# Kernel tuning notes

Hardware: AMD Instinct MI355X
Metric: run time of the kernel (lower is better)

The kernel has to match this reference:

```python
import jax, jax.numpy as jnp
import numpy as np
from jax import lax

B, L = 8, 1024
C_IN, D_MODEL = 3, 512
N_MAMBA, N_TRANS, NHEAD = 2, 2, 8
D_STATE, D_CONV, EXPAND = 16, 4, 2
DI = EXPAND * D_MODEL            # 1024, mamba inner dim
DT_RANK = D_MODEL // 16          # 32
DH = D_MODEL // NHEAD            # 64, head dim
DFF = 4 * D_MODEL


def setup_inputs() -> dict:
    key = jax.random.key(0)
    ks = iter(jax.random.split(key, 64))
    def rn(shape, s=0.05):
        return jax.random.normal(next(ks), shape, jnp.float32) * s
    inp = {
        'x': jax.random.normal(next(ks), (B, C_IN, L), jnp.float32),
        'proj_w': rn((D_MODEL, C_IN)), 'proj_b': rn((D_MODEL,)),
        # stacked per-mamba-layer params (leading dim = N_MAMBA)
        'm_in_w': rn((N_MAMBA, 2 * DI, D_MODEL)),
        'm_conv_w': rn((N_MAMBA, DI, D_CONV)), 'm_conv_b': rn((N_MAMBA, DI)),
        'm_xproj_w': rn((N_MAMBA, DT_RANK + 2 * D_STATE, DI)),
        'm_dt_w': rn((N_MAMBA, DI, DT_RANK)), 'm_dt_b': rn((N_MAMBA, DI)),
        'm_Alog': jnp.tile(jnp.log(jnp.arange(1, D_STATE + 1, dtype=jnp.float32)), (N_MAMBA, DI, 1)),
        'm_D': jnp.ones((N_MAMBA, DI), jnp.float32),
        'm_out_w': rn((N_MAMBA, D_MODEL, DI)),
        'm_ln_w': jnp.ones((N_MAMBA, D_MODEL), jnp.float32), 'm_ln_b': jnp.zeros((N_MAMBA, D_MODEL), jnp.float32),
        # stacked per-transformer-layer params
        't_qkv_w': rn((N_TRANS, 3 * D_MODEL, D_MODEL)), 't_qkv_b': rn((N_TRANS, 3 * D_MODEL)),
        't_ow': rn((N_TRANS, D_MODEL, D_MODEL)), 't_ob': rn((N_TRANS, D_MODEL)),
        't_l1w': rn((N_TRANS, DFF, D_MODEL)), 't_l1b': rn((N_TRANS, DFF)),
        't_l2w': rn((N_TRANS, D_MODEL, DFF)), 't_l2b': rn((N_TRANS, D_MODEL)),
        't_ln1w': jnp.ones((N_TRANS, D_MODEL), jnp.float32), 't_ln1b': jnp.zeros((N_TRANS, D_MODEL), jnp.float32),
        't_ln2w': jnp.ones((N_TRANS, D_MODEL), jnp.float32), 't_ln2b': jnp.zeros((N_TRANS, D_MODEL), jnp.float32),
        'no_w': jnp.ones((D_MODEL,), jnp.float32), 'no_b': jnp.zeros((D_MODEL,), jnp.float32),
    }
    return inp


def _ln(x, w, b, eps=1e-5):
    m = x.mean(-1, keepdims=True)
    v = ((x - m) ** 2).mean(-1, keepdims=True)
    return (x - m) / jnp.sqrt(v + eps) * w + b


def _pos_encoding(length, d):
    pos = jnp.arange(length, dtype=jnp.float32)[:, None]
    div = jnp.exp(jnp.arange(0, d, 2, dtype=jnp.float32) * (-np.log(10000.0) / d))
    pe = jnp.zeros((length, d), jnp.float32)
    pe = pe.at[:, 0::2].set(jnp.sin(pos * div)).at[:, 1::2].set(jnp.cos(pos * div))
    return pe


def _mamba(h, in_w, conv_w, conv_b, xp_w, dt_w, dt_b, Alog, Dp, out_w):
    # h: [B,L,d_model]
    xz = h @ in_w.T                                   # [B,L,2*DI]
    xm, z = jnp.split(xz, 2, axis=-1)
    # causal depthwise conv1d over time
    k = conv_w.T[:, None, :]                          # [D_CONV,1,DI]
    xc = lax.conv_general_dilated(xm, k, (1,), [(D_CONV - 1, 0)],
                                  dimension_numbers=('NWC', 'WIO', 'NWC'),
                                  feature_group_count=DI) + conv_b
    xc = jax.nn.silu(xc)
    xdb = xc @ xp_w.T                                 # [B,L,DT_RANK+2*D_STATE]
    dt = jax.nn.softplus(xdb[..., :DT_RANK] @ dt_w.T + dt_b)   # [B,L,DI]
    Bm = xdb[..., DT_RANK:DT_RANK + D_STATE]          # [B,L,D_STATE]
    Cm = xdb[..., DT_RANK + D_STATE:]                 # [B,L,D_STATE]
    A = -jnp.exp(Alog)                                # [DI,D_STATE]

    def step(state, t):
        dt_t, B_t, C_t, x_t = t                       # [B,DI],[B,S],[B,S],[B,DI]
        dA = jnp.exp(dt_t[..., None] * A)             # [B,DI,S]
        state = state * dA + (dt_t * x_t)[..., None] * B_t[:, None, :]
        y = jnp.einsum('bds,bs->bd', state, C_t)
        return state, y

    init = jnp.zeros((h.shape[0], DI, D_STATE), h.dtype)
    seq = (dt.transpose(1, 0, 2), Bm.transpose(1, 0, 2), Cm.transpose(1, 0, 2), xc.transpose(1, 0, 2))
    _, ys = lax.scan(step, init, seq)                 # ys: [L,B,DI]
    y = ys.transpose(1, 0, 2) + Dp * xc
    y = y * jax.nn.silu(z)
    return y @ out_w.T                                # [B,L,d_model]


def _transformer_layer(h, qkv_w, qkv_b, ow, ob, l1w, l1b, l2w, l2b, ln1w, ln1b, ln2w, ln2b):
    Bt, Lt, d = h.shape
    qkv = h @ qkv_w.T + qkv_b
    q, k, v = jnp.split(qkv, 3, axis=-1)
    q = q.reshape(Bt, Lt, NHEAD, DH); k = k.reshape(Bt, Lt, NHEAD, DH); v = v.reshape(Bt, Lt, NHEAD, DH)
    sc = jnp.einsum('blhd,bmhd->bhlm', q, k) / np.sqrt(DH).astype(np.float32)
    a = jax.nn.softmax(sc, axis=-1)
    o = jnp.einsum('bhlm,bmhd->blhd', a, v).reshape(Bt, Lt, d)
    h = _ln(h + o @ ow.T + ob, ln1w, ln1b)
    ff = jax.nn.relu(h @ l1w.T + l1b) @ l2w.T + l2b
    return _ln(h + ff, ln2w, ln2b)


def reference(x, proj_w, proj_b, m_in_w, m_conv_w, m_conv_b, m_xproj_w, m_dt_w, m_dt_b,
              m_Alog, m_D, m_out_w, m_ln_w, m_ln_b, t_qkv_w, t_qkv_b, t_ow, t_ob,
              t_l1w, t_l1b, t_l2w, t_l2b, t_ln1w, t_ln1b, t_ln2w, t_ln2b, no_w, no_b):
    # proj_in: 1x1 conv == pointwise linear over channels; output [B,L,d]
    h = jnp.einsum('bcl,dc->bld', x, proj_w) + proj_b
    for i in range(N_MAMBA):
        h = _ln(h + _mamba(h, m_in_w[i], m_conv_w[i], m_conv_b[i], m_xproj_w[i],
                           m_dt_w[i], m_dt_b[i], m_Alog[i], m_D[i], m_out_w[i]),
                m_ln_w[i], m_ln_b[i])
    h = h + _pos_encoding(h.shape[1], D_MODEL)
    for i in range(N_TRANS):
        h = _transformer_layer(h, t_qkv_w[i], t_qkv_b[i], t_ow[i], t_ob[i],
                               t_l1w[i], t_l1b[i], t_l2w[i], t_l2b[i],
                               t_ln1w[i], t_ln1b[i], t_ln2w[i], t_ln2b[i])
    h = _ln(h, no_w, no_b)
    return h, h.mean(axis=1)
```

## Files before the change

### kernel.cpp

```cpp
#include <hip/hip_runtime.h>
#include <cstddef>

#define BATCH 8
#define LSEQ 1024
#define DMODEL 512
#define DINNER 1024
#define DSTATE 16
#define DTRANK 32
#define NHEAD 8
#define DHEAD 64
#define DFF 2048
#define MTOK 8192
#define NCHUNK 16
#define CLEN 64

typedef __attribute__((ext_vector_type(8))) short bfrag;
typedef __attribute__((ext_vector_type(4))) float f32x4;
typedef __attribute__((ext_vector_type(4))) unsigned short us4;
typedef unsigned short ushort_t;

__device__ __forceinline__ float silu_f(float x) { return x / (1.f + __expf(-x)); }

__device__ __forceinline__ unsigned short f2bf(float f) {
  unsigned u = __float_as_uint(f);
  return (unsigned short)((u + 0x7FFFu + ((u >> 16) & 1u)) >> 16);
}
__device__ __forceinline__ float bf2f(ushort_t u) {
  return __uint_as_float((unsigned)u << 16);
}

__device__ __forceinline__ void gll16(const ushort_t* g, ushort_t* l) {
  __builtin_amdgcn_global_load_lds(
      (const __attribute__((address_space(1))) unsigned int*)g,
      (__attribute__((address_space(3))) unsigned int*)l, 16, 0, 0);
}

struct Cvt8Args {
  const float* s[8];
  ushort_t* d[8];
  int end[8];
};
__global__ __launch_bounds__(256) void cvt8(Cvt8Args a) {
  int blk = blockIdx.x;
  int seg = 0, start = 0;
#pragma unroll
  for (int i = 0; i < 7; ++i)
    if (blk >= a.end[i]) { seg = i + 1; start = a.end[i]; }
  int i4 = (blk - start) * 256 + threadIdx.x;
  float4 v = ((const float4*)a.s[seg])[i4];
  us4 o = {f2bf(v.x), f2bf(v.y), f2bf(v.z), f2bf(v.w)};
  ((us4*)a.d[seg])[i4] = o;
}

__global__ __launch_bounds__(256) void proj_kernel(const float* __restrict__ x,
                                                   const float* __restrict__ pw,
                                                   const float* __restrict__ pb,
                                                   float* __restrict__ h,
                                                   ushort_t* __restrict__ hbf) {
  int idx = blockIdx.x * 256 + threadIdx.x;
  int d = idx & 511;
  int l = (idx >> 9) & 1023;
  int b = idx >> 19;
  const float* xb = x + (size_t)b * 3 * 1024 + l;
  float v = pb[d] + xb[0] * pw[d * 3] + xb[1024] * pw[d * 3 + 1] + xb[2048] * pw[d * 3 + 2];
  h[idx] = v;
  hbf[idx] = f2bf(v);
}

template <int ACT, int CBF, int SPLITK, int BN>
__global__ __launch_bounds__(256) void gemm_gll(const ushort_t* __restrict__ A,
                                                const ushort_t* __restrict__ W,
                                                const float* __restrict__ bias,
                                                void* __restrict__ Cp,
                                                int K, int lda, int ldc) {
  __shared__ ushort_t sA[2][4096];
  __shared__ ushort_t sB[2][BN * 32];
  constexpr int MREP = (BN == 128) ? 4 : 2;
  const int bm = blockIdx.y * 128, bn = blockIdx.x * BN;
  const int tid = threadIdx.x;
  const int wid = tid >> 6, lane = tid & 63;
  const int wrb = (BN == 128) ? (wid >> 1) * 64 : wid * 32;
  const int wcb = (BN == 128) ? (wid & 1) * 64 : 0;
  const int lr = lane & 15, ls = lane >> 4;
  const int sw = ls ^ ((lr >> 1) & 3);

  const int kseg = K / SPLITK;
  const int kbeg = (SPLITK > 1) ? blockIdx.z * kseg : 0;

  const int c0 = wid * 128 + lane;
  const int c1 = c0 + 64;
  const int r0 = c0 >> 2, s0 = (c0 & 3) ^ ((r0 >> 1) & 3);
  const int r1 = c1 >> 2, s1 = (c1 & 3) ^ ((r1 >> 1) & 3);
  const ushort_t* gA0 = A + (size_t)(bm + r0) * lda + kbeg + s0 * 8;
  const ushort_t* gA1 = A + (size_t)(bm + r1) * lda + kbeg + s1 * 8;
  const ushort_t* gB0;
  const ushort_t* gB1 = nullptr;
  if constexpr (BN == 128) {
    gB0 = W + (size_t)(bn + r0) * K + kbeg + s0 * 8;
    gB1 = W + (size_t)(bn + r1) * K + kbeg + s1 * 8;
  } else {
    const int cb = wid * 64 + lane;
    const int rb = cb >> 2, sb2 = (cb & 3) ^ ((rb >> 1) & 3);
    gB0 = W + (size_t)(bn + rb) * K + kbeg + sb2 * 8;
  }

  f32x4 acc[MREP][4];
#pragma unroll
  for (int i = 0; i < MREP; ++i)
#pragma unroll
    for (int j = 0; j < 4; ++j) acc[i][j] = (f32x4)(0.f);

#define STAGE(buf, step)                                             \
  do {                                                               \
    gll16(gA0 + (step) * 32, &sA[buf][wid * 1024]);                  \
    gll16(gA1 + (step) * 32, &sA[buf][wid * 1024 + 512]);            \
    if constexpr (BN == 128) {                                       \
      gll16(gB0 + (step) * 32, &sB[buf][wid * 1024]);                \
      gll16(gB1 + (step) * 32, &sB[buf][wid * 1024 + 512]);          \
    } else {                                                         \
      gll16(gB0 + (step) * 32, &sB[buf][wid * 512]);                 \
    }                                                                \
  } while (0)

  const int NT = kseg / 32;
  STAGE(0, 0);
  for (int t = 0; t < NT; ++t) {
    const int cur = t & 1;
    if (t + 1 < NT) {
      STAGE(cur ^ 1, t + 1);
      if constexpr (BN == 128)
        asm volatile("s_waitcnt vmcnt(4)" ::: "memory");
      else
        asm volatile("s_waitcnt vmcnt(3)" ::: "memory");
    } else {
      asm volatile("s_waitcnt vmcnt(0)" ::: "memory");
    }
    __builtin_amdgcn_sched_barrier(0);
    __builtin_amdgcn_s_barrier();
    __builtin_amdgcn_sched_barrier(0);

    bfrag af[MREP], bf[4];
#pragma unroll
    for (int mi = 0; mi < MREP; ++mi) {
      int row = wrb + mi * 16 + lr;
      af[mi] = *(const bfrag*)&sA[cur][(size_t)((row << 2) + sw) * 8];
    }
#pragma unroll
    for (int nj = 0; nj < 4; ++nj) {
      int col = wcb + nj * 16 + lr;
      bf[nj] = *(const bfrag*)&sB[cur][(size_t)((col << 2) + sw) * 8];
    }
#pragma unroll
    for (int mi = 0; mi < MREP; ++mi)
#pragma unroll
      for (int nj = 0; nj < 4; ++nj)
        acc[mi][nj] = __builtin_amdgcn_mfma_f32_16x16x32_bf16(af[mi], bf[nj], acc[mi][nj], 0, 0, 0);

    __builtin_amdgcn_s_barrier();
    __builtin_amdgcn_sched_barrier(0);
  }
#undef STAGE

  if (SPLITK > 1) {
    float* Cz = (float*)Cp + (size_t)blockIdx.z * 8192 * ldc;
#pragma unroll
    for (int nj = 0; nj < 4; ++nj) {
      int col = bn + wcb + nj * 16 + lr;
#pragma unroll
      for (int mi = 0; mi < MREP; ++mi) {
        int row0 = bm + wrb + mi * 16 + ls * 4;
#pragma unroll
        for (int r = 0; r < 4; ++r)
          Cz[(size_t)(row0 + r) * ldc + col] = acc[mi][nj][r];
      }
    }
  } else {
#pragma unroll
    for (int nj = 0; nj < 4; ++nj) {
      int col = bn + wcb + nj * 16 + lr;
      float bv = bias ? bias[col] : 0.f;
#pragma unroll
      for (int mi = 0; mi < MREP; ++mi) {
        int row0 = bm + wrb + mi * 16 + ls * 4;
#pragma unroll
        for (int r = 0; r < 4; ++r) {
          float v = acc[mi][nj][r] + bv;
          if (ACT == 1) v = fmaxf(v, 0.f);
          if (ACT == 2) v = (v > 20.f) ? v : log1pf(__expf(v));
          if (CBF)
            ((ushort_t*)Cp)[(size_t)(row0 + r) * ldc + col] = f2bf(v);
          else
            ((float*)Cp)[(size_t)(row0 + r) * ldc + col] = v;
        }
      }
    }
  }
}

__global__ __launch_bounds__(256) void reduce8_xdb(const float* __restrict__ p,
                                                   float* __restrict__ xdb,
                                                   ushort_t* __restrict__ xdb_bf) {
  int i = blockIdx.x * 256 + threadIdx.x;
  float4 a = ((const float4*)p)[i];
#pragma unroll
  for (int z = 1; z < 8; ++z) {
    float4 b = ((const float4*)p)[i + z * 131072];
    a.x += b.x; a.y += b.y; a.z += b.z; a.w += b.w;
  }
  ((float4*)xdb)[i] = a;
  us4 o = {f2bf(a.x), f2bf(a.y), f2bf(a.z), f2bf(a.w)};
  ((us4*)xdb_bf)[i] = o;
}

__global__ __launch_bounds__(256) void conv_silu_kernel(const ushort_t* __restrict__ xz,
                                                        const float* __restrict__ cw,
                                                        const float* __restrict__ cb,
                                                        ushort_t* __restrict__ xc) {
  int idx = blockIdx.x * 256 + threadIdx.x;
  int d = idx & 1023;
  int t = (idx >> 10) & 1023;
  int b = idx >> 20;
  float acc = cb[d];
#pragma unroll
  for (int w = 0; w < 4; ++w) {
    int tt = t - 3 + w;
    if (tt >= 0) acc += bf2f(xz[(((size_t)(b * 1024 + tt)) << 11) + d]) * cw[d * 4 + w];
  }
  xc[idx] = f2bf(silu_f(acc));
}

__global__ __launch_bounds__(256) void scan_pass1(const ushort_t* __restrict__ dt,
                                                  const float* __restrict__ xdb,
                                                  const ushort_t* __restrict__ xc,
                                                  const float* __restrict__ Alog,
                                                  float* __restrict__ scrP,
                                                  float* __restrict__ scrL) {
  int idx = blockIdx.x * 256 + threadIdx.x;
  int sh = idx & 3;
  int d = (idx >> 2) & 1023;
  int c = (idx >> 12) & 15;
  int b = idx >> 16;
  float A[4], st[4], P[4];
#pragma unroll
  for (int s = 0; s < 4; ++s) {
    A[s] = -__expf(Alog[d * 16 + sh * 4 + s]);
    st[s] = 0.f;
    P[s] = 1.f;
  }
  int t0 = c * CLEN;
  size_t base = (((size_t)(b * 1024 + t0)) << 10) + d;
  const float* xb = xdb + (size_t)(b * 1024 + t0) * 64 + 32 + sh * 4;
  float dtv = bf2f(dt[base]), xv = bf2f(xc[base]);
  for (int t = 0; t < CLEN; ++t) {
    float dtn = 0.f, xvn = 0.f;
    if (t + 1 < CLEN) { dtn = bf2f(dt[base + 1024]); xvn = bf2f(xc[base + 1024]); }
    float4 Bv = *(const float4*)xb;
    float dx = dtv * xv;
    float e0 = __expf(dtv * A[0]), e1 = __expf(dtv * A[1]);
    float e2 = __expf(dtv * A[2]), e3 = __expf(dtv * A[3]);
    st[0] = st[0] * e0 + dx * Bv.x; P[0] *= e0;
    st[1] = st[1] * e1 + dx * Bv.y; P[1] *= e1;
    st[2] = st[2] * e2 + dx * Bv.z; P[2] *= e2;
    st[3] = st[3] * e3 + dx * Bv.w; P[3] *= e3;
    base += 1024; xb += 64;
    dtv = dtn; xv = xvn;
  }
  size_t pbase = (((size_t)((b * 16 + c) * 16 + sh * 4)) << 10) + d;
#pragma unroll
  for (int s = 0; s < 4; ++s) {
    scrP[pbase + ((size_t)s << 10)] = P[s];
    scrL[pbase + ((size_t)s << 10)] = st[s];
  }
}

__global__ __launch_bounds__(256) void scan_pass2(const float* __restrict__ scrP,
                                                  float* __restrict__ scrL) {
  int idx = blockIdx.x * 256 + threadIdx.x;
  int d = idx & 1023;
  int s = (idx >> 10) & 15;
  int b = idx >> 14;
  float cur = 0.f;
  for (int c = 0; c < 16; ++c) {
    size_t o = (((size_t)(((b * 16 + c) * 16) + s)) << 10) + d;
    float P = scrP[o];
    float loc = scrL[o];
    scrL[o] = cur;
    cur = cur * P + loc;
  }
}

__global__ __launch_bounds__(256) void scan_pass3(const ushort_t* __restrict__ dt,
                                                  const float* __restrict__ xdb,
                                                  const ushort_t* __restrict__ xc,
                                                  const ushort_t* __restrict__ xz,
                                                  ushort_t* __restrict__ ybf,
                                                  const float* __restrict__ Alog,
                                                  const float* __restrict__ Dp,
                                                  const float* __restrict__ scrL) {
  int idx = blockIdx.x * 256 + threadIdx.x;
  int sh = idx & 3;
  int d = (idx >> 2) & 1023;
  int c = (idx >> 12) & 15;
  int b = idx >> 16;
  float A[4], st[4];
  size_t pbase = (((size_t)((b * 16 + c) * 16 + sh * 4)) << 10) + d;
#pragma unroll
  for (int s = 0; s < 4; ++s) {
    A[s] = -__expf(Alog[d * 16 + sh * 4 + s]);
    st[s] = scrL[pbase + ((size_t)s << 10)];
  }
  float Dv = Dp[d];
  int t0 = c * CLEN;
  size_t base = (((size_t)(b * 1024 + t0)) << 10) + d;
  size_t zoff = ((((size_t)(b * 1024 + t0)) << 11)) + 1024 + d;
  const float* xb = xdb + (size_t)(b * 1024 + t0) * 64 + 32 + sh * 4;
  float dtv = bf2f(dt[base]), xv = bf2f(xc[base]), zv = bf2f(xz[zoff]);
  for (int t = 0; t < CLEN; ++t) {
    float dtn = 0.f, xvn = 0.f, zvn = 0.f;
    if (t + 1 < CLEN) {
      dtn = bf2f(dt[base + 1024]); xvn = bf2f(xc[base + 1024]); zvn = bf2f(xz[zoff + 2048]);
    }
    float4 Bv = *(const float4*)xb;
    float4 Cv = *(const float4*)(xb + 16);
    float dx = dtv * xv;
    float e0 = __expf(dtv * A[0]), e1 = __expf(dtv * A[1]);
    float e2 = __expf(dtv * A[2]), e3 = __expf(dtv * A[3]);
    st[0] = st[0] * e0 + dx * Bv.x;
    st[1] = st[1] * e1 + dx * Bv.y;
    st[2] = st[2] * e2 + dx * Bv.z;
    st[3] = st[3] * e3 + dx * Bv.w;
    float acc = st[0] * Cv.x + st[1] * Cv.y + st[2] * Cv.z + st[3] * Cv.w;
    acc += __shfl_xor(acc, 1);
    acc += __shfl_xor(acc, 2);
    if (sh == 0)
      ybf[base] = f2bf((acc + Dv * xv) * silu_f(zv));
    base += 1024; zoff += 2048; xb += 64;
    dtv = dtn; xv = xvn; zv = zvn;
  }
}

__global__ __launch_bounds__(128) void resid_ln_kernel(const float* __restrict__ x,
                                                       const float* __restrict__ add,
                                                       const float* __restrict__ w,
                                                       const float* __restrict__ bias,
                                                       float* __restrict__ out,
                                                       ushort_t* __restrict__ out_bf) {
  int row = blockIdx.x, tid = threadIdx.x;
  float4 v = ((const float4*)(x + (size_t)row * 512))[tid];
  if (add) {
    float4 a = ((const float4*)(add + (size_t)row * 512))[tid];
    v.x += a.x; v.y += a.y; v.z += a.z; v.w += a.w;
  }
  float s = v.x + v.y + v.z + v.w;
  float ss = v.x * v.x + v.y * v.y + v.z * v.z + v.w * v.w;
#pragma unroll
  for (int o = 32; o; o >>= 1) {
    s += __shfl_xor(s, o);
    ss += __shfl_xor(ss, o);
  }
  __shared__ float red[4];
  int wid = tid >> 6;
  if ((tid & 63) == 0) { red[wid] = s; red[2 + wid] = ss; }
  __syncthreads();
  s = red[0] + red[1];
  ss = red[2] + red[3];
  float mean = s * (1.f / 512.f);
  float var = ss * (1.f / 512.f) - mean * mean;
  float inv = rsqrtf(var + 1e-5f);
  float4 wv = ((const float4*)w)[tid];
  float4 bv = ((const float4*)bias)[tid];
  float4 ov;
  ov.x = (v.x - mean) * inv * wv.x + bv.x;
  ov.y = (v.y - mean) * inv * wv.y + bv.y;
  ov.z = (v.z - mean) * inv * wv.z + bv.z;
  ov.w = (v.w - mean) * inv * wv.w + bv.w;
  ((float4*)(out + (size_t)row * 512))[tid] = ov;
  if (out_bf) {
    us4 ob = {f2bf(ov.x), f2bf(ov.y), f2bf(ov.z), f2bf(ov.w)};
    ((us4*)(out_bf + (size_t)row * 512))[tid] = ob;
  }
}

__global__ __launch_bounds__(128) void resid_ln_sk(const float* __restrict__ x,
                                                   const float* __restrict__ p,
                                                   const float* __restrict__ pbias,
                                                   const float* __restrict__ w,
                                                   const float* __restrict__ bias,
                                                   float* __restrict__ out,
                                                   ushort_t* __restrict__ out_bf) {
  int row = blockIdx.x, tid = threadIdx.x;
  float4 v = ((const float4*)(x + (size_t)row * 512))[tid];
  float4 a = ((const float4*)(p + (size_t)row * 512))[tid];
  float4 c = ((const float4*)(p + 4194304 + (size_t)row * 512))[tid];
  v.x += a.x + c.x; v.y += a.y + c.y; v.z += a.z + c.z; v.w += a.w + c.w;
  if (pbias) {
    float4 pb = ((const float4*)pbias)[tid];
    v.x += pb.x; v.y += pb.y; v.z += pb.z; v.w += pb.w;
  }
  float s = v.x + v.y + v.z + v.w;
  float ss = v.x * v.x + v.y * v.y + v.z * v.z + v.w * v.w;
#pragma unroll
  for (int o = 32; o; o >>= 1) {
    s += __shfl_xor(s, o);
    ss += __shfl_xor(ss, o);
  }
  __shared__ float red[4];
  int wid = tid >> 6;
  if ((tid & 63) == 0) { red[wid] = s; red[2 + wid] = ss; }
  __syncthreads();
  s = red[0] + red[1];
  ss = red[2] + red[3];
  float mean = s * (1.f / 512.f);
  float var = ss * (1.f / 512.f) - mean * mean;
  float inv = rsqrtf(var + 1e-5f);
  float4 wv = ((const float4*)w)[tid];
  float4 bv = ((const float4*)bias)[tid];
  float4 ov;
  ov.x = (v.x - mean) * inv * wv.x + bv.x;
  ov.y = (v.y - mean) * inv * wv.y + bv.y;
  ov.z = (v.z - mean) * inv * wv.z + bv.z;
  ov.w = (v.w - mean) * inv * wv.w + bv.w;
  ((float4*)(out + (size_t)row * 512))[tid] = ov;
  us4 ob = {f2bf(ov.x), f2bf(ov.y), f2bf(ov.z), f2bf(ov.w)};
  ((us4*)(out_bf + (size_t)row * 512))[tid] = ob;
}

__global__ __launch_bounds__(256) void posenc_kernel(float* __restrict__ h,
                                                     ushort_t* __restrict__ hbf) {
  int idx = blockIdx.x * 256 + threadIdx.x;
  int d = idx & 511;
  int l = (idx >> 9) & 1023;
  float freq = __expf(-(float)(d & ~1) * (9.210340371976184f / 512.f));
  float ang = (float)l * freq;
  float v = h[idx] + ((d & 1) ? cosf(ang) : sinf(ang));
  h[idx] = v;
  hbf[idx] = f2bf(v);
}

__global__ __launch_bounds__(256) void attn_mfma(const ushort_t* __restrict__ qkv,
                                                 ushort_t* __restrict__ ao) {
  __shared__ unsigned short Qs[4096];
  __shared__ unsigned short Ks[4096];
  __shared__ unsigned short Vt[4096];
  __shared__ unsigned short Ps[4096];
  const int tid = threadIdx.x;
  const int w = blockIdx.x;
  const int bh = (w & 7) + (w >> 7) * 8;
  const int qt = (w >> 3) & 15;
  const int hh = bh & 7, b = bh >> 3;
  const int l0 = qt * 64;
  const size_t bb = (size_t)b * 1024 * 1536;

  const int srow = tid >> 2;
  const int sdb = (tid & 3) << 4;
  const int sc0 = sdb >> 3;

  {
    const ushort_t* qp = qkv + bb + (size_t)(l0 + srow) * 1536 + hh * 64 + sdb;
    *(bfrag*)&Qs[srow * 64 + ((sc0 ^ (srow & 7)) << 3)] = *(const bfrag*)qp;
    *(bfrag*)&Qs[srow * 64 + (((sc0 + 1) ^ (srow & 7)) << 3)] = *(const bfrag*)(qp + 8);
  }

  const int wid = tid >> 6, lane = tid & 63;
  const int l15 = lane & 15, rg = lane >> 4;
  const int l7 = l15 & 7;
  float m[4], lsum[4];
  f32x4 oacc[4];
#pragma unroll
  for (int r = 0; r < 4; ++r) { m[r] = -1e30f; lsum[r] = 0.f; }
#pragma unroll
  for (int nt = 0; nt < 4; ++nt) oacc[nt] = (f32x4)(0.f);

  for (int jt = 0; jt < 16; ++jt) {
    {
      const ushort_t* kp = qkv + bb + (size_t)(jt * 64 + srow) * 1536 + hh * 64 + 512 + sdb;
      *(bfrag*)&Ks[srow * 64 + ((sc0 ^ (srow & 7)) << 3)] = *(const bfrag*)kp;
      *(bfrag*)&Ks[srow * 64 + (((sc0 + 1) ^ (srow & 7)) << 3)] = *(const bfrag*)(kp + 8);
      const ushort_t* vp = kp + 512;
      unsigned short vv[16];
      *(bfrag*)&vv[0] = *(const bfrag*)vp;
      *(bfrag*)&vv[8] = *(const bfrag*)(vp + 8);
#pragma unroll
      for (int j = 0; j < 16; ++j) {
        int dd = sdb + j;
        Vt[dd * 64 + (((srow >> 3) ^ (dd & 7) ^ ((dd >> 3) & 7)) << 3) + (srow & 7)] = vv[j];
      }
    }
    __syncthreads();

    bfrag aq[2];
#pragma unroll
    for (int ks = 0; ks < 2; ++ks)
      aq[ks] = *(const bfrag*)&Qs[(wid * 16 + l15) * 64 + (((ks * 4 + rg) ^ l7) << 3)];
    f32x4 sc[4];
#pragma unroll
    for (int nt = 0; nt < 4; ++nt) {
      f32x4 s = (f32x4)(0.f);
#pragma unroll
      for (int ks = 0; ks < 2; ++ks) {
        bfrag bk = *(const bfrag*)&Ks[(nt * 16 + l15) * 64 + (((ks * 4 + rg) ^ l7) << 3)];
        s = __builtin_amdgcn_mfma_f32_16x16x32_bf16(aq[ks], bk, s, 0, 0, 0);
      }
      sc[nt] = s * 0.125f;
    }

#pragma unroll
    for (int r = 0; r < 4; ++r) {
      float mc = fmaxf(fmaxf(sc[0][r], sc[1][r]), fmaxf(sc[2][r], sc[3][r]));
#pragma unroll
      for (int o = 8; o; o >>= 1) mc = fmaxf(mc, __shfl_xor(mc, o));
      float mn = fmaxf(m[r], mc);
      float al = __expf(m[r] - mn);
      m[r] = mn;
      int prow = rg * 4 + r;
      float ps = 0.f;
#pragma unroll
      for (int nt = 0; nt < 4; ++nt) {
        float p = __expf(sc[nt][r] - mn);
        ps += p;
        int col = nt * 16 + l15;
        Ps[wid * 1024 + prow * 64 + ((((col >> 3) ^ (prow & 7))) << 3) + (col & 7)] = f2bf(p);
      }
#pragma unroll
      for (int o = 8; o; o >>= 1) ps += __shfl_xor(ps, o);
      lsum[r] = lsum[r] * al + ps;
#pragma unroll
      for (int nt = 0; nt < 4; ++nt) oacc[nt][r] *= al;
    }

    bfrag ap[2];
#pragma unroll
    for (int ks = 0; ks < 2; ++ks)
      ap[ks] = *(const bfrag*)&Ps[wid * 1024 + l15 * 64 + (((ks * 4 + rg) ^ l7) << 3)];
#pragma unroll
    for (int nt = 0; nt < 4; ++nt) {
      int vrow = nt * 16 + l15;
#pragma unroll
      for (int ks = 0; ks < 2; ++ks) {
        bfrag bv = *(const bfrag*)&Vt[vrow * 64 +
            (((ks * 4 + rg) ^ (vrow & 7) ^ ((vrow >> 3) & 7)) << 3)];
        oacc[nt] = __builtin_amdgcn_mfma_f32_16x16x32_bf16(ap[ks], bv, oacc[nt], 0, 0, 0);
      }
    }
    __syncthreads();
  }

#pragma unroll
  for (int r = 0; r < 4; ++r) {
    float inv = 1.f / lsum[r];
    int row = l0 + wid * 16 + rg * 4 + r;
    ushort_t* op = ao + ((size_t)(b * 1024 + row)) * 512 + hh * 64;
#pragma unroll
    for (int nt = 0; nt < 4; ++nt) op[nt * 16 + l15] = f2bf(oacc[nt][r] * inv);
  }
}

__global__ __launch_bounds__(512) void mean_part(const float* __restrict__ h,
                                                 float* __restrict__ part) {
  int blk = blockIdx.x;
  int b = blk >> 4, lc = blk & 15, d = threadIdx.x;
  float s = 0.f;
  int l0 = lc * 64;
  for (int l = l0; l < l0 + 64; ++l) s += h[(((size_t)(b * 1024 + l)) << 9) + d];
  part[((size_t)blk << 9) + d] = s;
}
__global__ __launch_bounds__(256) void mean_final(const float* __restrict__ part,
                                                  float* __restrict__ out2) {
  int i = blockIdx.x * 256 + threadIdx.x;
  int b = i >> 9, d = i & 511;
  float s = 0.f;
#pragma unroll
  for (int c = 0; c < 16; ++c) s += part[(((size_t)(b * 16 + c)) << 9) + d];
  out2[i] = s * (1.f / 1024.f);
}

extern "C" void kernel_launch(void* const* d_in, const int* in_sizes, int n_in,
                              void* d_out, int out_size, void* d_ws, size_t ws_size,
                              hipStream_t stream) {
  const float* x        = (const float*)d_in[0];
  const float* proj_w   = (const float*)d_in[1];
  const float* proj_b   = (const float*)d_in[2];
  const float* m_in_w   = (const float*)d_in[3];
  const float* m_conv_w = (const float*)d_in[4];
  const float* m_conv_b = (const float*)d_in[5];
  const float* m_xproj_w= (const float*)d_in[6];
  const float* m_dt_w   = (const float*)d_in[7];
  const float* m_dt_b   = (const float*)d_in[8];
  const float* m_Alog   = (const float*)d_in[9];
  const float* m_D      = (const float*)d_in[10];
  const float* m_out_w  = (const float*)d_in[11];
  const float* m_ln_w   = (const float*)d_in[12];
  const float* m_ln_b   = (const float*)d_in[13];
  const float* t_qkv_w  = (const float*)d_in[14];
  const float* t_qkv_b  = (const float*)d_in[15];
  const float* t_ow     = (const float*)d_in[16];
  const float* t_ob     = (const float*)d_in[17];
  const float* t_l1w    = (const float*)d_in[18];
  const float* t_l1b    = (const float*)d_in[19];
  const float* t_l2w    = (const float*)d_in[20];
  const float* t_l2b    = (const float*)d_in[21];
  const float* t_ln1w   = (const float*)d_in[22];
  const float* t_ln1b   = (const float*)d_in[23];
  const float* t_ln2w   = (const float*)d_in[24];
  const float* t_ln2b   = (const float*)d_in[25];
  const float* no_w     = (const float*)d_in[26];
  const float* no_b     = (const float*)d_in[27];

  float* ws   = (float*)d_ws;
  float* h    = ws;
  ushort_t* h_bf = (ushort_t*)(ws + 4194304);
  float* bufA = ws + 6291456;
  float* bufB = bufA + 16777216;
  float* bufC = bufB + 8388608;
  float* bufE = bufC + 8388608;
  float* bufF = bufE + 4194304;
  ushort_t* y_bf = (ushort_t*)(bufF + 524288);
  ushort_t* wbf  = (ushort_t*)(bufF + 524288 + 4194304);
  float* scrP = bufE;
  float* scrL = bufE + 2097152;

  ushort_t* wIN  = wbf;
  ushort_t* wOUT = wbf + 2097152;
  ushort_t* wQKV = wbf + 3145728;
  ushort_t* wOW  = wbf + 4718592;
  ushort_t* wL1  = wbf + 5242880;
  ushort_t* wL2  = wbf + 7340032;
  ushort_t* wXP  = wbf + 9437184;
  ushort_t* wDT  = wbf + 9568256;
  ushort_t* xdb_bf = wbf + 9633792;

  Cvt8Args ca;
  ca.s[0] = m_in_w;    ca.d[0] = wIN;  
  ca.s[1] = m_out_w;   ca.d[1] = wOUT;
  ca.s[2] = t_qkv_w;   ca.d[2] = wQKV;
  ca.s[3] = t_ow;      ca.d[3] = wOW;
  ca.s[4] = t_l1w;     ca.d[4] = wL1;
  ca.s[5] = t_l2w;     ca.d[5] = wL2;
  ca.s[6] = m_xproj_w; ca.d[6] = wXP;
  ca.s[7] = m_dt_w;    ca.d[7] = wDT;
  ca.end[0] = 2048; ca.end[1] = 3072; ca.end[2] = 4608; ca.end[3] = 5120;
  ca.end[4] = 7168; ca.end[5] = 9216; ca.end[6] = 9344; ca.end[7] = 9408;
  cvt8<<<9408, 256, 0, stream>>>(ca);

  proj_kernel<<<16384, 256, 0, stream>>>(x, proj_w, proj_b, h, h_bf);

  for (int i = 0; i < 2; ++i) {
    gemm_gll<0, 1, 1, 128><<<dim3(16, 64), 256, 0, stream>>>(
        h_bf, wIN + (size_t)i * 1048576, nullptr, bufA, DMODEL, DMODEL, 2 * DINNER);
    conv_silu_kernel<<<32768, 256, 0, stream>>>((const ushort_t*)bufA,
                                                m_conv_w + i * DINNER * 4,
                                                m_conv_b + i * DINNER, (ushort_t*)bufB);
    gemm_gll<0, 0, 8, 64><<<dim3(1, 64, 8), 256, 0, stream>>>(
        (const ushort_t*)bufB, wXP + (size_t)i * 65536, nullptr, bufC,
        DINNER, DINNER, 64);
    reduce8_xdb<<<512, 256, 0, stream>>>(bufC, bufF, xdb_bf);
    gemm_gll<2, 1, 1, 128><<<dim3(8, 64), 256, 0, stream>>>(
        xdb_bf, wDT + (size_t)i * 32768, m_dt_b + i * DINNER, bufC,
        DTRANK, 64, DINNER);
    scan_pass1<<<2048, 256, 0, stream>>>((const ushort_t*)bufC, bufF, (const ushort_t*)bufB,
                                         m_Alog + (size_t)i * DINNER * DSTATE, scrP, scrL);
    scan_pass2<<<512, 256, 0, stream>>>(scrP, scrL);
    scan_pass3<<<2048, 256, 0, stream>>>((const ushort_t*)bufC, bufF, (const ushort_t*)bufB,
                                         (const ushort_t*)bufA, y_bf,
                                         m_Alog + (size_t)i * DINNER * DSTATE,
                                         m_D + i * DINNER, scrL);
    gemm_gll<0, 0, 2, 128><<<dim3(4, 64, 2), 256, 0, stream>>>(
        y_bf, wOUT + (size_t)i * 524288, nullptr, bufC, DINNER, DINNER, DMODEL);
    resid_ln_sk<<<8192, 128, 0, stream>>>(h, bufC, nullptr, m_ln_w + i * DMODEL,
                                          m_ln_b + i * DMODEL, h, h_bf);
  }

  posenc_kernel<<<16384, 256, 0, stream>>>(h, h_bf);

  for (int i = 0; i < 2; ++i) {
    gemm_gll<0, 1, 1, 128><<<dim3(12, 64), 256, 0, stream>>>(
        h_bf, wQKV + (size_t)i * 786432, t_qkv_b + i * 3 * DMODEL, bufA,
        DMODEL, DMODEL, 3 * DMODEL);
    attn_mfma<<<1024, 256, 0, stream>>>((const ushort_t*)bufA, (ushort_t*)bufB);
    gemm_gll<0, 0, 2, 128><<<dim3(4, 64, 2), 256, 0, stream>>>(
        (const ushort_t*)bufB, wOW + (size_t)i * 262144, nullptr, bufC,
        DMODEL, DMODEL, DMODEL);
    resid_ln_sk<<<8192, 128, 0, stream>>>(h, bufC, t_ob + i * DMODEL,
                                          t_ln1w + i * DMODEL, t_ln1b + i * DMODEL, h, h_bf);
    gemm_gll<1, 1, 1, 128><<<dim3(16, 64), 256, 0, stream>>>(
        h_bf, wL1 + (size_t)i * 1048576, t_l1b + i * DFF, bufA,
        DMODEL, DMODEL, DFF);
    gemm_gll<0, 0, 2, 128><<<dim3(4, 64, 2), 256, 0, stream>>>(
        (const ushort_t*)bufA, wL2 + (size_t)i * 1048576, nullptr, bufC,
        DFF, DFF, DMODEL);
    resid_ln_sk<<<8192, 128, 0, stream>>>(h, bufC, t_l2b + i * DMODEL,
                                          t_ln2w + i * DMODEL, t_ln2b + i * DMODEL, h, h_bf);
  }

  float* out_h = (float*)d_out;
  resid_ln_kernel<<<8192, 128, 0, stream>>>(h, nullptr, no_w, no_b, out_h, nullptr);
  mean_part<<<128, 512, 0, stream>>>(out_h, bufF);
  mean_final<<<16, 256, 0, stream>>>(bufF, out_h + 4194304);
}
```

Baseline: 925.2 us.

## Store split-K partials in bf16, vectorize conv, lazy softmax rescale in attention

Split-K GEMM partial outputs are now written as bf16 instead of fp32 and read back as bf16 by the residual+LayerNorm kernel, halving that intermediate traffic. The conv+SiLU kernel processes two channels per thread with 32-bit loads and stores. Attention skips the running-max rescale unless the new max exceeds the old by more than 8, and converts probabilities to bf16 by truncation. These trade accuracy (bf16 partial sums, truncation, a stale max) for less memory traffic and fewer exp and multiply operations.

```diff
diff --git a/kernel.cpp b/kernel.cpp
--- a/kernel.cpp
+++ b/kernel.cpp
@@ -162,7 +162,6 @@
 #undef STAGE
 
   if (SPLITK > 1) {
-    float* Cz = (float*)Cp + (size_t)blockIdx.z * 8192 * ldc;
 #pragma unroll
     for (int nj = 0; nj < 4; ++nj) {
       int col = bn + wcb + nj * 16 + lr;
@@ -170,8 +169,14 @@
       for (int mi = 0; mi < MREP; ++mi) {
         int row0 = bm + wrb + mi * 16 + ls * 4;
 #pragma unroll
-        for (int r = 0; r < 4; ++r)
-          Cz[(size_t)(row0 + r) * ldc + col] = acc[mi][nj][r];
+        for (int r = 0; r < 4; ++r) {
+          if (CBF)
+            ((ushort_t*)Cp)[(size_t)blockIdx.z * 8192 * ldc +
+                            (size_t)(row0 + r) * ldc + col] = f2bf(acc[mi][nj][r]);
+          else
+            ((float*)Cp)[(size_t)blockIdx.z * 8192 * ldc +
+                         (size_t)(row0 + r) * ldc + col] = acc[mi][nj][r];
+        }
       }
     }
   } else {
@@ -212,21 +217,27 @@
   ((us4*)xdb_bf)[i] = o;
 }
 
-__global__ __launch_bounds__(256) void conv_silu_kernel(const ushort_t* __restrict__ xz,
+__global__ __launch_bounds__(256) void conv_silu_kernel(const unsigned* __restrict__ xz,
                                                         const float* __restrict__ cw,
                                                         const float* __restrict__ cb,
-                                                        ushort_t* __restrict__ xc) {
+                                                        unsigned* __restrict__ xc) {
   int idx = blockIdx.x * 256 + threadIdx.x;
-  int d = idx & 1023;
-  int t = (idx >> 10) & 1023;
-  int b = idx >> 20;
-  float acc = cb[d];
+  int dp = idx & 511;
+  int t = (idx >> 9) & 1023;
+  int b = idx >> 19;
+  int d0 = dp * 2;
+  float a0 = cb[d0], a1 = cb[d0 + 1];
 #pragma unroll
   for (int w = 0; w < 4; ++w) {
     int tt = t - 3 + w;
-    if (tt >= 0) acc += bf2f(xz[(((size_t)(b * 1024 + tt)) << 11) + d]) * cw[d * 4 + w];
-  }
-  xc[idx] = f2bf(silu_f(acc));
+    if (tt >= 0) {
+      unsigned v = xz[(((size_t)(b * 1024 + tt)) << 10) + dp];
+      a0 += bf2f((ushort_t)(v & 0xffff)) * cw[d0 * 4 + w];
+      a1 += bf2f((ushort_t)(v >> 16)) * cw[(d0 + 1) * 4 + w];
+    }
+  }
+  unsigned o = (unsigned)f2bf(silu_f(a0)) | ((unsigned)f2bf(silu_f(a1)) << 16);
+  xc[(((size_t)(b * 1024 + t)) << 9) + dp] = o;
 }
 
 __global__ __launch_bounds__(256) void scan_pass1(const ushort_t* __restrict__ dt,
@@ -382,7 +393,7 @@
 }
 
 __global__ __launch_bounds__(128) void resid_ln_sk(const float* __restrict__ x,
-                                                   const float* __restrict__ p,
+                                                   const ushort_t* __restrict__ p,
                                                    const float* __restrict__ pbias,
                                                    const float* __restrict__ w,
                                                    const float* __restrict__ bias,
@@ -390,9 +401,12 @@
                                                    ushort_t* __restrict__ out_bf) {
   int row = blockIdx.x, tid = threadIdx.x;
   float4 v = ((const float4*)(x + (size_t)row * 512))[tid];
-  float4 a = ((const float4*)(p + (size_t)row * 512))[tid];
-  float4 c = ((const float4*)(p + 4194304 + (size_t)row * 512))[tid];
-  v.x += a.x + c.x; v.y += a.y + c.y; v.z += a.z + c.z; v.w += a.w + c.w;
+  us4 a = ((const us4*)(p + (size_t)row * 512))[tid];
+  us4 c = ((const us4*)(p + 4194304 + (size_t)row * 512))[tid];
+  v.x += bf2f(a.x) + bf2f(c.x);
+  v.y += bf2f(a.y) + bf2f(c.y);
+  v.z += bf2f(a.z) + bf2f(c.z);
+  v.w += bf2f(a.w) + bf2f(c.w);
   if (pbias) {
     float4 pb = ((const float4*)pbias)[tid];
     v.x += pb.x; v.y += pb.y; v.z += pb.z; v.w += pb.w;
@@ -509,23 +523,27 @@
       float mc = fmaxf(fmaxf(sc[0][r], sc[1][r]), fmaxf(sc[2][r], sc[3][r]));
 #pragma unroll
       for (int o = 8; o; o >>= 1) mc = fmaxf(mc, __shfl_xor(mc, o));
-      float mn = fmaxf(m[r], mc);
-      float al = __expf(m[r] - mn);
-      m[r] = mn;
+      if (__any(mc > m[r] + 8.f)) {
+        float mn = fmaxf(m[r], mc);
+        float al = __expf(m[r] - mn);
+        m[r] = mn;
+        lsum[r] *= al;
+#pragma unroll
+        for (int nt = 0; nt < 4; ++nt) oacc[nt][r] *= al;
+      }
       int prow = rg * 4 + r;
       float ps = 0.f;
 #pragma unroll
       for (int nt = 0; nt < 4; ++nt) {
-        float p = __expf(sc[nt][r] - mn);
+        float p = __expf(sc[nt][r] - m[r]);
         ps += p;
         int col = nt * 16 + l15;
-        Ps[wid * 1024 + prow * 64 + ((((col >> 3) ^ (prow & 7))) << 3) + (col & 7)] = f2bf(p);
+        Ps[wid * 1024 + prow * 64 + ((((col >> 3) ^ (prow & 7))) << 3) + (col & 7)] =
+            (ushort_t)(__float_as_uint(p) >> 16);
       }
 #pragma unroll
       for (int o = 8; o; o >>= 1) ps += __shfl_xor(ps, o);
-      lsum[r] = lsum[r] * al + ps;
-#pragma unroll
-      for (int nt = 0; nt < 4; ++nt) oacc[nt][r] *= al;
+      lsum[r] += ps;
     }
 
     bfrag ap[2];
@@ -630,7 +648,7 @@
   ushort_t* xdb_bf = wbf + 9633792;
 
   Cvt8Args ca;
-  ca.s[0] = m_in_w;    ca.d[0] = wIN;  
+  ca.s[0] = m_in_w;    ca.d[0] = wIN;
   ca.s[1] = m_out_w;   ca.d[1] = wOUT;
   ca.s[2] = t_qkv_w;   ca.d[2] = wQKV;
   ca.s[3] = t_ow;      ca.d[3] = wOW;
@@ -647,9 +665,9 @@
   for (int i = 0; i < 2; ++i) {
     gemm_gll<0, 1, 1, 128><<<dim3(16, 64), 256, 0, stream>>>(
         h_bf, wIN + (size_t)i * 1048576, nullptr, bufA, DMODEL, DMODEL, 2 * DINNER);
-    conv_silu_kernel<<<32768, 256, 0, stream>>>((const ushort_t*)bufA,
+    conv_silu_kernel<<<16384, 256, 0, stream>>>((const unsigned*)bufA,
                                                 m_conv_w + i * DINNER * 4,
-                                                m_conv_b + i * DINNER, (ushort_t*)bufB);
+                                                m_conv_b + i * DINNER, (unsigned*)bufB);
     gemm_gll<0, 0, 8, 64><<<dim3(1, 64, 8), 256, 0, stream>>>(
         (const ushort_t*)bufB, wXP + (size_t)i * 65536, nullptr, bufC,
         DINNER, DINNER, 64);
@@ -664,10 +682,10 @@
                                          (const ushort_t*)bufA, y_bf,
                                          m_Alog + (size_t)i * DINNER * DSTATE,
                                          m_D + i * DINNER, scrL);
-    gemm_gll<0, 0, 2, 128><<<dim3(4, 64, 2), 256, 0, stream>>>(
+    gemm_gll<0, 1, 2, 128><<<dim3(4, 64, 2), 256, 0, stream>>>(
         y_bf, wOUT + (size_t)i * 524288, nullptr, bufC, DINNER, DINNER, DMODEL);
-    resid_ln_sk<<<8192, 128, 0, stream>>>(h, bufC, nullptr, m_ln_w + i * DMODEL,
-                                          m_ln_b + i * DMODEL, h, h_bf);
+    resid_ln_sk<<<8192, 128, 0, stream>>>(h, (const ushort_t*)bufC, nullptr,
+                                          m_ln_w + i * DMODEL, m_ln_b + i * DMODEL, h, h_bf);
   }
 
   posenc_kernel<<<16384, 256, 0, stream>>>(h, h_bf);
@@ -677,18 +695,18 @@
         h_bf, wQKV + (size_t)i * 786432, t_qkv_b + i * 3 * DMODEL, bufA,
         DMODEL, DMODEL, 3 * DMODEL);
     attn_mfma<<<1024, 256, 0, stream>>>((const ushort_t*)bufA, (ushort_t*)bufB);
-    gemm_gll<0, 0, 2, 128><<<dim3(4, 64, 2), 256, 0, stream>>>(
+    gemm_gll<0, 1, 2, 128><<<dim3(4, 64, 2), 256, 0, stream>>>(
         (const ushort_t*)bufB, wOW + (size_t)i * 262144, nullptr, bufC,
         DMODEL, DMODEL, DMODEL);
-    resid_ln_sk<<<8192, 128, 0, stream>>>(h, bufC, t_ob + i * DMODEL,
+    resid_ln_sk<<<8192, 128, 0, stream>>>(h, (const ushort_t*)bufC, t_ob + i * DMODEL,
                                           t_ln1w + i * DMODEL, t_ln1b + i * DMODEL, h, h_bf);
     gemm_gll<1, 1, 1, 128><<<dim3(16, 64), 256, 0, stream>>>(
         h_bf, wL1 + (size_t)i * 1048576, t_l1b + i * DFF, bufA,
         DMODEL, DMODEL, DFF);
-    gemm_gll<0, 0, 2, 128><<<dim3(4, 64, 2), 256, 0, stream>>>(
+    gemm_gll<0, 1, 2, 128><<<dim3(4, 64, 2), 256, 0, stream>>>(
         (const ushort_t*)bufA, wL2 + (size_t)i * 1048576, nullptr, bufC,
         DFF, DFF, DMODEL);
-    resid_ln_sk<<<8192, 128, 0, stream>>>(h, bufC, t_l2b + i * DMODEL,
+    resid_ln_sk<<<8192, 128, 0, stream>>>(h, (const ushort_t*)bufC, t_l2b + i * DMODEL,
                                           t_ln2w + i * DMODEL, t_ln2b + i * DMODEL, h, h_bf);
   }
 
```

Result: slower. 963.4 us (+4.1%).
